# Performance work log

Hardware: AMD Instinct MI355X
Metric: run time of the kernel (lower is better)

Reference implementation:

```python
import jax, jax.numpy as jnp
import numpy as np

B, C, N_OUT = 8, 64, 65536
N_IN = 262144  # unpooled (input) spatial size
K, P = 9, 4    # kernel_size, bilinear interp points


def setup_inputs() -> dict:
    key = jax.random.key(0)
    k1, k2, k3, k4 = jax.random.split(key, 4)
    x = jax.random.normal(k1, (B, C, N_OUT), dtype=jnp.float32)
    idx_mask = jax.random.randint(k2, (B, C, N_OUT), 0, K, dtype=jnp.int32)
    sample_map = jax.random.randint(k3, (N_OUT, K, P), 0, N_IN, dtype=jnp.int32)
    interp_weights = jax.random.uniform(k4, (N_OUT, K, P), dtype=jnp.float32)
    return {"x": x, "idx_mask": idx_mask, "sample_map": sample_map,
            "interp_weights": interp_weights}


def reference(x, idx_mask, sample_map, interp_weights):
    # x: [B,C,N_out] pooled values; idx_mask: [B,C,N_out] winning kernel tap
    # sample_map: [N_out,K,P] int indices into flattened unpooled domain
    # interp_weights: [N_out,K,P] interpolation weights
    b, c, n_out = x.shape
    o_idx = jnp.arange(n_out)[None, None, :]               # [1,1,N_out]
    sel_map = sample_map[o_idx, idx_mask]                  # [B,C,N_out,P]
    sel_w = interp_weights[o_idx, idx_mask]                # [B,C,N_out,P]
    contrib = sel_w * x[..., None]                         # [B,C,N_out,P]
    out = jnp.zeros((b, c, N_IN), dtype=x.dtype)
    bi = jnp.arange(b)[:, None, None, None]
    ci = jnp.arange(c)[None, :, None, None]
    out = out.at[bi, ci, sel_map].add(contrib)             # scatter-add unpool
    return out
```

## Files before the change

### kernel.cpp

```cpp
#include <hip/hip_runtime.h>

#define BB      8
#define CC      64
#define N_OUT   65536
#define N_IN    262144
#define KK      9
#define PP      4
#define NE      (N_OUT * KK * PP)
#define NPLANES 512
#define CHUNK   16
#define NCHUNKS (N_IN / CHUNK)
#define NKEY    NCHUNKS
#define GTH     512
#define NS      (GTH / 32)
#define NFB     256
#define EPB     (NE / NFB)

typedef float f4_t __attribute__((ext_vector_type(4)));

#define WS_OFFSETS 0
#define WS_TOT     16400
#define WS_PRIV    32784
#define WS_HDR     (32784 + NFB * NKEY)
#define WS_ENTR    (4227088 + N_OUT * KK)
#define WS_XK      (4816912 + 2 * NE)
#define WS_END     (9535504 + N_OUT * 512)

#define XKTILE 16
#define XPAD   520
__global__ __launch_bounds__(256) void k_xk(const float* __restrict__ x,
                                            const int*   __restrict__ idx,
                                            unsigned* __restrict__ xk,
                                            unsigned* __restrict__ hdr) {
    __shared__ float xs[XKTILE * XPAD];
    __shared__ unsigned char ks[XKTILE * XPAD];
    __shared__ unsigned ot[XKTILE * 512];
    __shared__ int cnt[XKTILE][12];
    __shared__ int cur[XKTILE][12];
    const int t = threadIdx.x;
    const int obase = blockIdx.x * XKTILE;

    for (int i = t; i < XKTILE * 12; i += 256) cnt[i / 12][i % 12] = 0;

    for (int i = t; i < 512 * (XKTILE / 4); i += 256) {
        int p = i >> 2, q = i & 3;
        const size_t g = (size_t)p * N_OUT + obase + 4 * q;
        float4 xv = *(const float4*)(x + g);
        int4   kv = *(const int4*)(idx + g);
        int b = (4 * q) * XPAD + p;
        xs[b] = xv.x; xs[b + XPAD] = xv.y; xs[b + 2 * XPAD] = xv.z; xs[b + 3 * XPAD] = xv.w;
        ks[b] = (unsigned char)kv.x; ks[b + XPAD] = (unsigned char)kv.y;
        ks[b + 2 * XPAD] = (unsigned char)kv.z; ks[b + 3 * XPAD] = (unsigned char)kv.w;
    }
    __syncthreads();
    for (int i = t; i < XKTILE * 512; i += 256) {
        int oo = i >> 9, p = i & 511;
        atomicAdd(&cnt[oo][ks[oo * XPAD + p]], 1);
    }
    __syncthreads();
    if (t < XKTILE) {
        int s = 0;
        for (int k = 0; k < KK; ++k) {
            int c = cnt[t][k];
            cur[t][k] = s;
            hdr[(size_t)(obase + t) * KK + k] = (unsigned)(s | (c << 16));
            s += c;
        }
    }
    __syncthreads();
    for (int i = t; i < XKTILE * 512; i += 256) {
        int oo = i >> 9, p = i & 511;
        int k = ks[oo * XPAD + p];
        int pos = atomicAdd(&cur[oo][k], 1);
        unsigned xb = __float_as_uint(xs[oo * XPAD + p]);
        ot[(oo << 9) + pos] = (xb & 0xFFFFFE00u) | (unsigned)p;
    }
    __syncthreads();
    for (int i = t; i < XKTILE * 128; i += 256) {
        int oo = i >> 7, c4 = i & 127;
        ((int4*)(xk + (((size_t)(obase + oo)) << 9)))[c4] = ((const int4*)(ot + (oo << 9)))[c4];
    }
}

__global__ __launch_bounds__(1024) void k_histA(const int* __restrict__ smap,
                                                int* __restrict__ priv) {
    __shared__ unsigned h32[NKEY / 2];
    const int b = blockIdx.x;
    const int t = threadIdx.x;
    for (int i = t; i < NKEY / 2; i += 1024) h32[i] = 0u;
    __syncthreads();
    const int e0 = b * EPB;
    #pragma unroll 3
    for (int i = 0; i < EPB / 1024; ++i) {
        const int key = smap[e0 + i * 1024 + t] >> 4;
        atomicAdd(&h32[key >> 1], 1u << ((key & 1) << 4));
    }
    __syncthreads();
    for (int i = t; i < NKEY; i += 1024)
        priv[b * NKEY + i] = (int)((h32[i >> 1] >> ((i & 1) << 4)) & 0xFFFFu);
}

__global__ __launch_bounds__(1024) void k_colscan(int* __restrict__ priv,
                                                  int* __restrict__ tot) {
    const int key = blockIdx.x * 1024 + threadIdx.x;
    int run = 0;
    for (int b = 0; b < NFB; ++b) {
        int* p = priv + b * NKEY + key;
        int v = *p; *p = run; run += v;
    }
    tot[key] = run;
}

__global__ __launch_bounds__(1024) void k_scan16k(const int* __restrict__ tot,
                                                  int* __restrict__ offsets) {
    __shared__ int sw[1024];
    const int t = threadIdx.x;
    int4 q0 = ((const int4*)tot)[4 * t + 0];
    int4 q1 = ((const int4*)tot)[4 * t + 1];
    int4 q2 = ((const int4*)tot)[4 * t + 2];
    int4 q3 = ((const int4*)tot)[4 * t + 3];
    int vals[16] = {q0.x, q0.y, q0.z, q0.w, q1.x, q1.y, q1.z, q1.w,
                    q2.x, q2.y, q2.z, q2.w, q3.x, q3.y, q3.z, q3.w};
    int s = 0;
    #pragma unroll
    for (int i = 0; i < 16; ++i) s += vals[i];
    sw[t] = s;
    __syncthreads();
    for (int off = 1; off < 1024; off <<= 1) {
        int v = (t >= off) ? sw[t - off] : 0;
        __syncthreads();
        sw[t] += v;
        __syncthreads();
    }
    int run = sw[t] - s;
    int o[16];
    #pragma unroll
    for (int i = 0; i < 16; ++i) { o[i] = run; run += vals[i]; }
    ((int4*)offsets)[4 * t + 0] = make_int4(o[0], o[1], o[2], o[3]);
    ((int4*)offsets)[4 * t + 1] = make_int4(o[4], o[5], o[6], o[7]);
    ((int4*)offsets)[4 * t + 2] = make_int4(o[8], o[9], o[10], o[11]);
    ((int4*)offsets)[4 * t + 3] = make_int4(o[12], o[13], o[14], o[15]);
    if (t == 1023) offsets[NKEY] = NE;
}

__global__ __launch_bounds__(1024) void k_fillB(const int* __restrict__ smap,
                                                const float* __restrict__ wts,
                                                const int* __restrict__ priv,
                                                const int* __restrict__ offsets,
                                                const unsigned* __restrict__ hdr,
                                                int2* __restrict__ entries) {
    __shared__ int cur[NKEY];
    const int b = blockIdx.x;
    const int t = threadIdx.x;
    for (int i = t; i < NKEY; i += 1024) cur[i] = offsets[i] + priv[b * NKEY + i];
    __syncthreads();
    const int e0 = b * EPB;
    #pragma unroll 3
    for (int i = 0; i < EPB / 1024; ++i) {
        const int e = e0 + i * 1024 + t;
        const int n = smap[e];
        const int o = e / 36;
        const int r = e - o * 36;
        const int k = r >> 2;
        const unsigned h = hdr[(size_t)o * KK + k];
        const int st = (int)(h & 0xFFFFu);
        const int cn = (int)(h >> 16);
        const unsigned wb = (__float_as_uint(wts[e]) + 0x8000u) >> 16;
        const int pos = atomicAdd(&cur[n >> 4], 1);
        entries[pos] = make_int2((o << 16) | ((n & 15) << 12) | ((cn - 1) << 2),
                                 (int)((wb << 16) | (unsigned)st));
    }
}

#define DECODE(e, o, nl, cn, st, w)                         \
    const int o  = ((unsigned)(e).x) >> 16;                 \
    const int nl = ((e).x >> 12) & 15;                      \
    const int cn = (((e).x >> 2) & 511) + 1;                \
    const int st = (e).y & 0xFFFF;                          \
    const float w = __uint_as_float(((unsigned)(e).y >> 16) << 16);

#define SWZ(p, nl) ((p) ^ ((nl) << 1))
__global__ __launch_bounds__(GTH, 8) void k_gather7(const int* __restrict__ offsets,
                                                    const int2* __restrict__ entries,
                                                    const unsigned* __restrict__ xk,
                                                    float* __restrict__ out) {
    __shared__ float acc[CHUNK * NPLANES];
    const int bid = blockIdx.x;
    const int c = (bid & 7) * (NCHUNKS / 8) + (bid >> 3);
    const int tid = threadIdx.x;
    const int l32 = tid & 31;
    const int sid = tid >> 5;

    f4_t* a4 = (f4_t*)acc;
    for (int i = tid; i < CHUNK * NPLANES / 4; i += GTH) a4[i] = (f4_t){0.f, 0.f, 0.f, 0.f};
    __syncthreads();

    const int j1 = offsets[c + 1];
    int jA = offsets[c] + sid;

    int2 eA = {0, 0}, eB = {0, 0}, eC = {0, 0};
    unsigned xA0 = 0, xA1 = 0, xB0 = 0, xB1 = 0;

    if (jA < j1) eA = entries[jA];
    int jB = jA + NS;
    if (jB < j1) eB = entries[jB];
    if (jA < j1) {
        DECODE(eA, o, nl, cn, st, w)
        const unsigned* r = xk + ((size_t)o << 9) + st;
        if (l32 < cn)      xA0 = r[l32];
        if (l32 + 32 < cn) xA1 = r[l32 + 32];
    }
    if (jB < j1) {
        DECODE(eB, o, nl, cn, st, w)
        const unsigned* r = xk + ((size_t)o << 9) + st;
        if (l32 < cn)      xB0 = r[l32];
        if (l32 + 32 < cn) xB1 = r[l32 + 32];
    }
    int jC = jB + NS;
    if (jC < j1) eC = entries[jC];

    while (jA < j1) {
        unsigned xC0 = 0, xC1 = 0;
        if (jC < j1) {
            DECODE(eC, o, nl, cn, st, w)
            const unsigned* r = xk + ((size_t)o << 9) + st;
            if (l32 < cn)      xC0 = r[l32];
            if (l32 + 32 < cn) xC1 = r[l32 + 32];
        }
        const int jD = jC + NS;
        int2 eD = {0, 0};
        if (jD < j1) eD = entries[jD];

        {
            DECODE(eA, o, nl, cn, st, w)
            if (l32 < cn)
                atomicAdd(&acc[(nl << 9) + SWZ((int)(xA0 & 511), nl)],
                          w * __uint_as_float(xA0 & 0xFFFFFE00u));
            if (l32 + 32 < cn)
                atomicAdd(&acc[(nl << 9) + SWZ((int)(xA1 & 511), nl)],
                          w * __uint_as_float(xA1 & 0xFFFFFE00u));
            if (cn > 64) {
                const unsigned* r = xk + ((size_t)o << 9) + st;
                for (int bb = l32 + 64; bb < cn; bb += 32) {
                    unsigned u = r[bb];
                    atomicAdd(&acc[(nl << 9) + SWZ((int)(u & 511), nl)],
                              w * __uint_as_float(u & 0xFFFFFE00u));
                }
            }
        }
        eA = eB; xA0 = xB0; xA1 = xB1; jA = jB;
        eB = eC; xB0 = xC0; xB1 = xC1; jB = jC;
        eC = eD; jC = jD;
    }
    __syncthreads();

    const int n0 = c << 4;
    for (int i = tid; i < CHUNK * NPLANES / 4; i += GTH) {
        const int p = i >> 2;
        const int nl = (i & 3) << 2;
        float4 v;
        v.x = acc[((nl + 0) << 9) + SWZ(p, nl + 0)];
        v.y = acc[((nl + 1) << 9) + SWZ(p, nl + 1)];
        v.z = acc[((nl + 2) << 9) + SWZ(p, nl + 2)];
        v.w = acc[((nl + 3) << 9) + SWZ(p, nl + 3)];
        *(float4*)(out + (size_t)p * N_IN + n0 + nl) = v;
    }
}

__global__ __launch_bounds__(256) void zero_kernel(float4* __restrict__ out, int n4) {
    int i = blockIdx.x * blockDim.x + threadIdx.x;
    int stride = gridDim.x * blockDim.x;
    const float4 z = {0.f, 0.f, 0.f, 0.f};
    for (; i < n4; i += stride) out[i] = z;
}

__global__ __launch_bounds__(256) void scatter_kernel(
    const float* __restrict__ x, const int* __restrict__ idx_mask,
    const int4* __restrict__ smap, const float4* __restrict__ wts,
    float* __restrict__ out)
{
    const int plane = blockIdx.x >> 8;
    const int o = ((blockIdx.x & 255) << 8) + threadIdx.x;
    const long ibase = (long)plane * N_OUT + o;
    const float xv = x[ibase];
    const int k = idx_mask[ibase];
    const int row = o * KK + k;
    const int4 m = smap[row];
    const float4 w = wts[row];
    float* op = out + (long)plane * N_IN;
    atomicAdd(op + m.x, w.x * xv);
    atomicAdd(op + m.y, w.y * xv);
    atomicAdd(op + m.z, w.z * xv);
    atomicAdd(op + m.w, w.w * xv);
}

extern "C" void kernel_launch(void* const* d_in, const int* in_sizes, int n_in,
                              void* d_out, int out_size, void* d_ws, size_t ws_size,
                              hipStream_t stream) {
    const float* x    = (const float*)d_in[0];
    const int*   idx  = (const int*)d_in[1];
    const int*   smap = (const int*)d_in[2];
    const float* wts  = (const float*)d_in[3];
    float* out = (float*)d_out;

    if (ws_size < (size_t)WS_END * 4) {
        zero_kernel<<<4096, 256, 0, stream>>>((float4*)out, out_size / 4);
        scatter_kernel<<<NPLANES * (N_OUT / 256), 256, 0, stream>>>(
            x, idx, (const int4*)smap, (const float4*)wts, out);
        return;
    }

    int* ws = (int*)d_ws;
    int* offsets   = ws + WS_OFFSETS;
    int* tot       = ws + WS_TOT;
    int* priv      = ws + WS_PRIV;
    unsigned* hdr  = (unsigned*)(ws + WS_HDR);
    int2* entries  = (int2*)(ws + WS_ENTR);
    unsigned* xk   = (unsigned*)(ws + WS_XK);

    k_xk<<<N_OUT / XKTILE, 256, 0, stream>>>(x, idx, xk, hdr);
    k_histA<<<NFB, 1024, 0, stream>>>(smap, priv);
    k_colscan<<<16, 1024, 0, stream>>>(priv, tot);
    k_scan16k<<<1, 1024, 0, stream>>>(tot, offsets);
    k_fillB<<<NFB, 1024, 0, stream>>>(smap, wts, priv, offsets, hdr, entries);

    k_gather7<<<NCHUNKS, GTH, 0, stream>>>(offsets, entries, xk, out);
}
```

Measured before the change: 966.0 us.

## Double gather chunk size to 32 and stage bucket entries in LDS

Buckets the unpooled domain in chunks of 32 positions instead of 16. This halves the number of gather blocks and the histogram/scan sizes, and each block now writes 128-byte contiguous output runs per plane. The gather kernel preloads up to 512 bucket entries into shared memory with nontemporal loads, stores output nontemporally, and simplifies the entry prefetch pipeline and swizzle. The per-block LDS accumulator doubles to 64 KB, so occupancy drops (launch bound now 4 blocks per CU) and shared-atomic contention on the larger tile may change.

```diff
diff --git a/kernel.cpp b/kernel.cpp
--- a/kernel.cpp
+++ b/kernel.cpp
@@ -8,23 +8,24 @@
 #define PP      4
 #define NE      (N_OUT * KK * PP)
 #define NPLANES 512
-#define CHUNK   16
+#define CHUNK   32
 #define NCHUNKS (N_IN / CHUNK)
 #define NKEY    NCHUNKS
 #define GTH     512
 #define NS      (GTH / 32)
 #define NFB     256
 #define EPB     (NE / NFB)
+#define ENT_STAGE 512
 
 typedef float f4_t __attribute__((ext_vector_type(4)));
 
 #define WS_OFFSETS 0
-#define WS_TOT     16400
-#define WS_PRIV    32784
-#define WS_HDR     (32784 + NFB * NKEY)
-#define WS_ENTR    (4227088 + N_OUT * KK)
-#define WS_XK      (4816912 + 2 * NE)
-#define WS_END     (9535504 + N_OUT * 512)
+#define WS_TOT     8208
+#define WS_PRIV    16400
+#define WS_HDR     (16400 + NFB * NKEY)
+#define WS_ENTR    (2113552 + N_OUT * KK)
+#define WS_XK      (2703376 + 2 * NE)
+#define WS_END     (7421968 + N_OUT * 512)
 
 #define XKTILE 16
 #define XPAD   520
@@ -92,7 +93,7 @@
     const int e0 = b * EPB;
     #pragma unroll 3
     for (int i = 0; i < EPB / 1024; ++i) {
-        const int key = smap[e0 + i * 1024 + t] >> 4;
+        const int key = smap[e0 + i * 1024 + t] >> 5;
         atomicAdd(&h32[key >> 1], 1u << ((key & 1) << 4));
     }
     __syncthreads();
@@ -111,19 +112,13 @@
     tot[key] = run;
 }
 
-__global__ __launch_bounds__(1024) void k_scan16k(const int* __restrict__ tot,
-                                                  int* __restrict__ offsets) {
+__global__ __launch_bounds__(1024) void k_scan8k(const int* __restrict__ counts,
+                                                 int* __restrict__ offsets) {
     __shared__ int sw[1024];
     const int t = threadIdx.x;
-    int4 q0 = ((const int4*)tot)[4 * t + 0];
-    int4 q1 = ((const int4*)tot)[4 * t + 1];
-    int4 q2 = ((const int4*)tot)[4 * t + 2];
-    int4 q3 = ((const int4*)tot)[4 * t + 3];
-    int vals[16] = {q0.x, q0.y, q0.z, q0.w, q1.x, q1.y, q1.z, q1.w,
-                    q2.x, q2.y, q2.z, q2.w, q3.x, q3.y, q3.z, q3.w};
-    int s = 0;
-    #pragma unroll
-    for (int i = 0; i < 16; ++i) s += vals[i];
+    int4 a = ((const int4*)counts)[2 * t];
+    int4 b = ((const int4*)counts)[2 * t + 1];
+    int s = a.x + a.y + a.z + a.w + b.x + b.y + b.z + b.w;
     sw[t] = s;
     __syncthreads();
     for (int off = 1; off < 1024; off <<= 1) {
@@ -133,13 +128,12 @@
         __syncthreads();
     }
     int run = sw[t] - s;
-    int o[16];
+    int vals[8] = {a.x, a.y, a.z, a.w, b.x, b.y, b.z, b.w};
+    int o[8];
     #pragma unroll
-    for (int i = 0; i < 16; ++i) { o[i] = run; run += vals[i]; }
-    ((int4*)offsets)[4 * t + 0] = make_int4(o[0], o[1], o[2], o[3]);
-    ((int4*)offsets)[4 * t + 1] = make_int4(o[4], o[5], o[6], o[7]);
-    ((int4*)offsets)[4 * t + 2] = make_int4(o[8], o[9], o[10], o[11]);
-    ((int4*)offsets)[4 * t + 3] = make_int4(o[12], o[13], o[14], o[15]);
+    for (int q = 0; q < 8; ++q) { o[q] = run; run += vals[q]; }
+    ((int4*)offsets)[2 * t]     = make_int4(o[0], o[1], o[2], o[3]);
+    ((int4*)offsets)[2 * t + 1] = make_int4(o[4], o[5], o[6], o[7]);
     if (t == 1023) offsets[NKEY] = NE;
 }
 
@@ -166,25 +160,31 @@
         const int st = (int)(h & 0xFFFFu);
         const int cn = (int)(h >> 16);
         const unsigned wb = (__float_as_uint(wts[e]) + 0x8000u) >> 16;
-        const int pos = atomicAdd(&cur[n >> 4], 1);
-        entries[pos] = make_int2((o << 16) | ((n & 15) << 12) | ((cn - 1) << 2),
+        const int pos = atomicAdd(&cur[n >> 5], 1);
+        entries[pos] = make_int2((o << 16) | ((n & 31) << 11) | ((cn - 1) << 2),
                                  (int)((wb << 16) | (unsigned)st));
     }
 }
 
 #define DECODE(e, o, nl, cn, st, w)                         \
     const int o  = ((unsigned)(e).x) >> 16;                 \
-    const int nl = ((e).x >> 12) & 15;                      \
+    const int nl = ((e).x >> 11) & 31;                      \
     const int cn = (((e).x >> 2) & 511) + 1;                \
     const int st = (e).y & 0xFFFF;                          \
     const float w = __uint_as_float(((unsigned)(e).y >> 16) << 16);
 
-#define SWZ(p, nl) ((p) ^ ((nl) << 1))
-__global__ __launch_bounds__(GTH, 8) void k_gather7(const int* __restrict__ offsets,
+__device__ __forceinline__ int2 get_ent(const int2* __restrict__ gent,
+                                        const int2* __restrict__ lent, int j) {
+    return (j < ENT_STAGE) ? lent[j] : gent[j];
+}
+
+#define SWZ(p, nl) ((p) ^ (nl))
+__global__ __launch_bounds__(GTH, 4) void k_gather8(const int* __restrict__ offsets,
                                                     const int2* __restrict__ entries,
                                                     const unsigned* __restrict__ xk,
                                                     float* __restrict__ out) {
     __shared__ float acc[CHUNK * NPLANES];
+    __shared__ int2 ent[ENT_STAGE];
     const int bid = blockIdx.x;
     const int c = (bid & 7) * (NCHUNKS / 8) + (bid >> 3);
     const int tid = threadIdx.x;
@@ -193,44 +193,50 @@
 
     f4_t* a4 = (f4_t*)acc;
     for (int i = tid; i < CHUNK * NPLANES / 4; i += GTH) a4[i] = (f4_t){0.f, 0.f, 0.f, 0.f};
-    __syncthreads();
-
+
+    const int j0 = offsets[c];
     const int j1 = offsets[c + 1];
-    int jA = offsets[c] + sid;
-
-    int2 eA = {0, 0}, eB = {0, 0}, eC = {0, 0};
+    const int je = j1 - j0;
+    const int2* gent = entries + j0;
+    {
+        const int n2 = min(je, ENT_STAGE) * 2;
+        const int* src = (const int*)gent;
+        int* dst = (int*)ent;
+        for (int i = tid; i < n2; i += GTH) dst[i] = __builtin_nontemporal_load(src + i);
+    }
+    __syncthreads();
+
+    int jA = sid;
+    int2 eA = {0, 0}, eB = {0, 0};
     unsigned xA0 = 0, xA1 = 0, xB0 = 0, xB1 = 0;
 
-    if (jA < j1) eA = entries[jA];
-    int jB = jA + NS;
-    if (jB < j1) eB = entries[jB];
-    if (jA < j1) {
+    if (jA < je) {
+        eA = get_ent(gent, ent, jA);
         DECODE(eA, o, nl, cn, st, w)
         const unsigned* r = xk + ((size_t)o << 9) + st;
         if (l32 < cn)      xA0 = r[l32];
         if (l32 + 32 < cn) xA1 = r[l32 + 32];
     }
-    if (jB < j1) {
+    int jB = jA + NS;
+    if (jB < je) {
+        eB = get_ent(gent, ent, jB);
         DECODE(eB, o, nl, cn, st, w)
         const unsigned* r = xk + ((size_t)o << 9) + st;
         if (l32 < cn)      xB0 = r[l32];
         if (l32 + 32 < cn) xB1 = r[l32 + 32];
     }
     int jC = jB + NS;
-    if (jC < j1) eC = entries[jC];
-
-    while (jA < j1) {
+
+    while (jA < je) {
         unsigned xC0 = 0, xC1 = 0;
-        if (jC < j1) {
+        int2 eC = {0, 0};
+        if (jC < je) {
+            eC = get_ent(gent, ent, jC);
             DECODE(eC, o, nl, cn, st, w)
             const unsigned* r = xk + ((size_t)o << 9) + st;
             if (l32 < cn)      xC0 = r[l32];
             if (l32 + 32 < cn) xC1 = r[l32 + 32];
         }
-        const int jD = jC + NS;
-        int2 eD = {0, 0};
-        if (jD < j1) eD = entries[jD];
-
         {
             DECODE(eA, o, nl, cn, st, w)
             if (l32 < cn)
@@ -250,20 +256,20 @@
         }
         eA = eB; xA0 = xB0; xA1 = xB1; jA = jB;
         eB = eC; xB0 = xC0; xB1 = xC1; jB = jC;
-        eC = eD; jC = jD;
-    }
-    __syncthreads();
-
-    const int n0 = c << 4;
+        jC += NS;
+    }
+    __syncthreads();
+
+    const int n0 = c << 5;
     for (int i = tid; i < CHUNK * NPLANES / 4; i += GTH) {
-        const int p = i >> 2;
-        const int nl = (i & 3) << 2;
-        float4 v;
+        const int p = i >> 3;
+        const int nl = (i & 7) << 2;
+        f4_t v;
         v.x = acc[((nl + 0) << 9) + SWZ(p, nl + 0)];
         v.y = acc[((nl + 1) << 9) + SWZ(p, nl + 1)];
         v.z = acc[((nl + 2) << 9) + SWZ(p, nl + 2)];
         v.w = acc[((nl + 3) << 9) + SWZ(p, nl + 3)];
-        *(float4*)(out + (size_t)p * N_IN + n0 + nl) = v;
+        __builtin_nontemporal_store(v, (f4_t*)(out + (size_t)p * N_IN + n0 + nl));
     }
 }
 
@@ -320,9 +326,9 @@
 
     k_xk<<<N_OUT / XKTILE, 256, 0, stream>>>(x, idx, xk, hdr);
     k_histA<<<NFB, 1024, 0, stream>>>(smap, priv);
-    k_colscan<<<16, 1024, 0, stream>>>(priv, tot);
-    k_scan16k<<<1, 1024, 0, stream>>>(tot, offsets);
+    k_colscan<<<8, 1024, 0, stream>>>(priv, tot);
+    k_scan8k<<<1, 1024, 0, stream>>>(tot, offsets);
     k_fillB<<<NFB, 1024, 0, stream>>>(smap, wts, priv, offsets, hdr, entries);
 
-    k_gather7<<<NCHUNKS, GTH, 0, stream>>>(offsets, entries, xk, out);
-}
+    k_gather8<<<NCHUNKS, GTH, 0, stream>>>(offsets, entries, xk, out);
+}
```

Result: no change. 957.0 us (-0.9%).
